# Performance work log

Measured on AMD Instinct MI355X. Metric: run time of the kernel, lower is better.

The kernel has to match this reference:

```python
import jax, jax.numpy as jnp
import numpy as np

N = 100000
E = 1600000
D_IN = 128
HEADS = 8
HEAD_DIM = 16  # hidden_channels // heads = 128 // 8
D_HID = HEADS * HEAD_DIM  # 128
D_OUT = 128
NEG_SLOPE = 0.2


def setup_inputs() -> dict:
    key = jax.random.key(0)
    ks = jax.random.split(key, 10)
    x = jax.random.normal(ks[0], (N, D_IN), dtype=jnp.float32)
    edge_index = jax.random.randint(ks[1], (2, E), 0, N, dtype=jnp.int64)
    s = 1.0 / np.sqrt(D_IN)
    W_gat = jax.random.uniform(ks[2], (D_IN, D_HID), minval=-s, maxval=s, dtype=jnp.float32)
    att_src = jax.random.uniform(ks[3], (HEADS, HEAD_DIM), minval=-s, maxval=s, dtype=jnp.float32)
    att_dst = jax.random.uniform(ks[4], (HEADS, HEAD_DIM), minval=-s, maxval=s, dtype=jnp.float32)
    b_gat = jnp.zeros((D_HID,), dtype=jnp.float32)
    so = 1.0 / np.sqrt(D_OUT)
    W_fc1 = jax.random.uniform(ks[5], (D_OUT, D_OUT), minval=-so, maxval=so, dtype=jnp.float32)
    b_fc1 = jax.random.uniform(ks[6], (D_OUT,), minval=-so, maxval=so, dtype=jnp.float32)
    W_fc2 = jax.random.uniform(ks[7], (D_OUT, D_OUT), minval=-so, maxval=so, dtype=jnp.float32)
    b_fc2 = jax.random.uniform(ks[8], (D_OUT,), minval=-so, maxval=so, dtype=jnp.float32)
    return {"x": x, "edge_index": edge_index, "W_gat": W_gat, "att_src": att_src,
            "att_dst": att_dst, "b_gat": b_gat, "W_fc1": W_fc1, "b_fc1": b_fc1,
            "W_fc2": W_fc2, "b_fc2": b_fc2}


def _gat_conv(x, src, dst, W_gat, att_src, att_dst, b_gat):
    n = x.shape[0]
    xp = (x @ W_gat).reshape(n, HEADS, HEAD_DIM)        # [N,H,C]
    a_src = jnp.einsum('nhc,hc->nh', xp, att_src)       # [N,H]
    a_dst = jnp.einsum('nhc,hc->nh', xp, att_dst)       # [N,H]
    e = jax.nn.leaky_relu(a_src[src] + a_dst[dst], NEG_SLOPE)  # [E,H]
    # segment softmax over edges grouped by destination node
    e_max = jax.ops.segment_max(e, dst, num_segments=n)
    e = jnp.exp(e - e_max[dst])
    e_sum = jax.ops.segment_sum(e, dst, num_segments=n)
    alpha = e / (e_sum[dst] + 1e-16)                    # [E,H]
    msg = xp[src] * alpha[:, :, None]                   # [E,H,C]
    out = jax.ops.segment_sum(msg, dst, num_segments=n) # [N,H,C]
    return out.reshape(n, D_HID) + b_gat


def reference(x, edge_index, W_gat, att_src, att_dst, b_gat, W_fc1, b_fc1, W_fc2, b_fc2):
    n = x.shape[0]
    # PyG GATConv default add_self_loops=True
    loops = jnp.arange(n, dtype=edge_index.dtype)
    src = jnp.concatenate([edge_index[0], loops])
    dst = jnp.concatenate([edge_index[1], loops])
    z = _gat_conv(x, src, dst, W_gat, att_src, att_dst, b_gat)
    z1 = z @ W_fc1 + b_fc1
    z2 = z @ W_fc2 + b_fc2
    return (z, z1, z2)
```

## Files before the change

kernel.cpp:

```cpp
#include <hip/hip_runtime.h>
#include <hip/hip_bf16.h>


#define NBUCK  256
#define BSHIFT 9
#define BNODES 512
#define IPB    8192

typedef __attribute__((ext_vector_type(8))) short bf16x8;
typedef __attribute__((ext_vector_type(4))) float f32x4;

static __device__ __forceinline__ short f2bf(float f) {
    __hip_bfloat16 h = __float2bfloat16(f);
    return *reinterpret_cast<short*>(&h);
}

__global__ __launch_bounds__(256) void k0_swizzle(
    const float* __restrict__ W0, const float* __restrict__ W1,
    const float* __restrict__ W2, const float* __restrict__ att_s,
    const float* __restrict__ att_d, unsigned short* __restrict__ S0,
    unsigned short* __restrict__ S1, unsigned short* __restrict__ S2,
    unsigned short* __restrict__ Sa)
{
    const int t = blockIdx.x * 256 + threadIdx.x;
    if (t < 3 * 2048) {
        const int m = t >> 11;
        const int r = t & 2047;
        const int tile = r >> 6;
        const int l    = r & 63;
        const int ks   = tile & 3;
        const int cb   = tile >> 2;
        const int c    = cb * 16 + (l & 15);
        const int kb   = ks * 32 + (l >> 4) * 8;
        const float* W = (m == 0) ? W0 : (m == 1) ? W1 : W2;
        unsigned short* S = (m == 0) ? S0 : (m == 1) ? S1 : S2;
        unsigned short* dst = S + ((size_t)tile * 64 + l) * 8;
#pragma unroll
        for (int j = 0; j < 8; ++j)
            dst[j] = (unsigned short)f2bf(W[(kb + j) * 128 + c]);
    } else if (t < 3 * 2048 + 256) {
        const int r  = t - 3 * 2048;
        const int ks = r >> 6;
        const int l  = r & 63;
        const int hp = l & 15;
        const int h  = hp & 7;
        const float* av = (hp < 8) ? (att_s + h * 16) : (att_d + h * 16);
        unsigned short* dst = Sa + ((size_t)ks * 64 + l) * 8;
#pragma unroll
        for (int j = 0; j < 8; ++j) {
            const int k = ks * 32 + (l >> 4) * 8 + j;
            float acc = 0.f;
#pragma unroll
            for (int u = 0; u < 16; ++u)
                acc += W0[k * 128 + h * 16 + u] * av[u];
            dst[j] = (unsigned short)f2bf(acc);
        }
    }
}

__global__ __launch_bounds__(256) void g1_mfma(
    const float* __restrict__ x, const unsigned short* __restrict__ Wswz,
    const unsigned short* __restrict__ Sa, unsigned short* __restrict__ xpb,
    float* __restrict__ a_src, float* __restrict__ a_dst, int n)
{
    const int wid  = __builtin_amdgcn_readfirstlane(threadIdx.x >> 6);
    const int lane = threadIdx.x & 63;
    const int lr   = lane & 15;
    const int kg   = lane >> 4;
    const int rowbase = blockIdx.x * 128 + wid * 32;

    bf16x8 afr[2][4];
#pragma unroll
    for (int rt = 0; rt < 2; ++rt) {
        int row = rowbase + rt * 16 + lr;
        row = (row < n) ? row : (n - 1);
        const float* rp = x + (size_t)row * 128 + kg * 8;
#pragma unroll
        for (int ks = 0; ks < 4; ++ks) {
            const float4 v0 = *reinterpret_cast<const float4*>(rp + ks * 32);
            const float4 v1 = *reinterpret_cast<const float4*>(rp + ks * 32 + 4);
            bf16x8 a;
            a[0] = f2bf(v0.x); a[1] = f2bf(v0.y); a[2] = f2bf(v0.z); a[3] = f2bf(v0.w);
            a[4] = f2bf(v1.x); a[5] = f2bf(v1.y); a[6] = f2bf(v1.z); a[7] = f2bf(v1.w);
            afr[rt][ks] = a;
        }
    }

    f32x4 acc[2][8] = {};
#pragma unroll
    for (int cb = 0; cb < 8; ++cb) {
        const unsigned short* bp = Wswz + ((size_t)(cb * 4) * 64 + lane) * 8;
        bf16x8 bfr[4];
#pragma unroll
        for (int ks = 0; ks < 4; ++ks)
            bfr[ks] = *reinterpret_cast<const bf16x8*>(bp + (size_t)ks * 512);
#pragma unroll
        for (int ks = 0; ks < 4; ++ks) {
            acc[0][cb] = __builtin_amdgcn_mfma_f32_16x16x32_bf16(afr[0][ks], bfr[ks], acc[0][cb], 0, 0, 0);
            acc[1][cb] = __builtin_amdgcn_mfma_f32_16x16x32_bf16(afr[1][ks], bfr[ks], acc[1][cb], 0, 0, 0);
        }
    }

    f32x4 accs[2] = {};
#pragma unroll
    for (int ks = 0; ks < 4; ++ks) {
        const bf16x8 bs = *reinterpret_cast<const bf16x8*>(Sa + ((size_t)ks * 64 + lane) * 8);
        accs[0] = __builtin_amdgcn_mfma_f32_16x16x32_bf16(afr[0][ks], bs, accs[0], 0, 0, 0);
        accs[1] = __builtin_amdgcn_mfma_f32_16x16x32_bf16(afr[1][ks], bs, accs[1], 0, 0, 0);
    }

#pragma unroll
    for (int rt = 0; rt < 2; ++rt) {
#pragma unroll
        for (int reg = 0; reg < 4; ++reg) {
            const int row = rowbase + rt * 16 + kg * 4 + reg;
            if (row < n) {
                unsigned short* op = xpb + (size_t)row * 128 + lr;
#pragma unroll
                for (int cb = 0; cb < 8; ++cb)
                    op[cb * 16] = (unsigned short)f2bf(acc[rt][cb][reg]);
                if (lr < 8) a_src[row * 8 + lr] = accs[rt][reg];
                else        a_dst[row * 8 + (lr - 8)] = accs[rt][reg];
            }
        }
    }
}

__global__ __launch_bounds__(256) void p1_hist(
    const int* __restrict__ ei, int* __restrict__ M, int E, int N, int nblk)
{
    __shared__ int h[NBUCK];
    const int tid = threadIdx.x;
    for (int k = tid; k < NBUCK; k += 256) h[k] = 0;
    __syncthreads();

    const int tot = E + N;
    const int base = blockIdx.x * IPB;
    const int lim = (base + IPB < tot) ? base + IPB : tot;
    for (int j = base + tid; j < lim; j += 256) {
        const int d = (j < E) ? ei[E + j] : (j - E);
        atomicAdd(&h[d >> BSHIFT], 1);
    }
    __syncthreads();
    for (int k = tid; k < NBUCK; k += 256)
        M[(size_t)k * nblk + blockIdx.x] = h[k];
}

__global__ __launch_bounds__(256) void p2a_colscan(
    int* __restrict__ M, int* __restrict__ col_total, int nblk)
{
    const int b    = blockIdx.x;
    const int tid  = threadIdx.x;
    const int lane = tid & 63;
    const int wid  = tid >> 6;
    __shared__ int wsum[4];

    int carry = 0;
    for (int base = 0; base < nblk; base += 256) {
        const int idx = base + tid;
        const int v = (idx < nblk) ? M[(size_t)b * nblk + idx] : 0;
        int ws = v;
#pragma unroll
        for (int off = 1; off < 64; off <<= 1) {
            const int t = __shfl_up(ws, off);
            if (lane >= off) ws += t;
        }
        if (lane == 63) wsum[wid] = ws;
        __syncthreads();
        int woff = 0;
        for (int w2 = 0; w2 < wid; ++w2) woff += wsum[w2];
        const int alltot = wsum[0] + wsum[1] + wsum[2] + wsum[3];
        if (idx < nblk) M[(size_t)b * nblk + idx] = carry + woff + ws - v;
        carry += alltot;
        __syncthreads();
    }
    if (tid == 0) col_total[b] = carry;
}

__global__ __launch_bounds__(NBUCK) void p2b_bucketptr(
    const int* __restrict__ col_total, int* __restrict__ bucket_ptr,
    int* __restrict__ row_ptr, int N)
{
    const int tid  = threadIdx.x;
    const int lane = tid & 63;
    const int wid  = tid >> 6;
    __shared__ int wsum[4];

    const int v = col_total[tid];
    int ws = v;
#pragma unroll
    for (int off = 1; off < 64; off <<= 1) {
        const int t = __shfl_up(ws, off);
        if (lane >= off) ws += t;
    }
    if (lane == 63) wsum[wid] = ws;
    __syncthreads();
    int woff = 0;
    for (int w2 = 0; w2 < wid; ++w2) woff += wsum[w2];
    const int excl = woff + ws - v;
    bucket_ptr[tid] = excl;
    if (tid == NBUCK - 1) {
        bucket_ptr[NBUCK] = excl + v;
        row_ptr[N] = excl + v;
    }
}

__global__ __launch_bounds__(256) void p3_scatter(
    const int* __restrict__ ei, const int* __restrict__ M,
    const int* __restrict__ bucket_ptr, int* __restrict__ pairs,
    int E, int N, int nblk)
{
    __shared__ int lcnt[NBUCK];
    const int tid = threadIdx.x;
    for (int k = tid; k < NBUCK; k += 256) lcnt[k] = 0;
    __syncthreads();

    const int tot = E + N;
    const int base = blockIdx.x * IPB;
    const int lim = (base + IPB < tot) ? base + IPB : tot;
    for (int j = base + tid; j < lim; j += 256) {
        int s, d;
        if (j < E) { s = ei[j]; d = ei[E + j]; }
        else       { s = j - E; d = s; }
        const int b = d >> BSHIFT;
        const int r = atomicAdd(&lcnt[b], 1);
        const int pos = bucket_ptr[b] + M[(size_t)b * nblk + blockIdx.x] + r;
        pairs[pos] = s | ((d & (BNODES - 1)) << 17);
    }
}

__global__ __launch_bounds__(256) void p4_finalize(
    const int* __restrict__ pairs, const int* __restrict__ bucket_ptr,
    int* __restrict__ row_ptr, int* __restrict__ csr_src, int N)
{
    const int b     = blockIdx.x;
    const int node0 = b << BSHIFT;
    const int beg   = bucket_ptr[b];
    const int end   = bucket_ptr[b + 1];
    const int tid   = threadIdx.x;
    const int lane  = tid & 63;
    const int wid   = tid >> 6;

    __shared__ int hist[BNODES];
    __shared__ int exc[BNODES];
    __shared__ int cnt2[BNODES];
    __shared__ int wsum[4];

    for (int k = tid; k < BNODES; k += 256) { hist[k] = 0; cnt2[k] = 0; }
    __syncthreads();

    for (int i = beg + tid; i < end; i += 256)
        atomicAdd(&hist[pairs[i] >> 17], 1);
    __syncthreads();

    const int a0 = hist[2 * tid];
    const int a1 = hist[2 * tid + 1];
    const int s  = a0 + a1;
    int ws = s;
#pragma unroll
    for (int off = 1; off < 64; off <<= 1) {
        const int t = __shfl_up(ws, off);
        if (lane >= off) ws += t;
    }
    if (lane == 63) wsum[wid] = ws;
    __syncthreads();
    int woff = 0;
    for (int w2 = 0; w2 < wid; ++w2) woff += wsum[w2];
    const int e0 = woff + ws - s;
    exc[2 * tid]     = e0;
    exc[2 * tid + 1] = e0 + a0;
    __syncthreads();

    for (int k = tid; k < BNODES; k += 256) {
        const int node = node0 + k;
        if (node < N) row_ptr[node] = beg + exc[k];
    }
    for (int i = beg + tid; i < end; i += 256) {
        const int v  = pairs[i];
        const int dl = v >> 17;
        const int r  = atomicAdd(&cnt2[dl], 1);
        csr_src[beg + exc[dl] + r] = v & 0x1FFFF;
    }
}

__global__ __launch_bounds__(256) void k5_aggregate(
    const unsigned short* __restrict__ xpb, const float* __restrict__ a_src,
    const float* __restrict__ a_dst, const int* __restrict__ row_ptr,
    const int* __restrict__ csr_src, const float* __restrict__ b_gat,
    float* __restrict__ z, unsigned int* __restrict__ zb, int n)
{
    const int wave = blockIdx.x * 4 + __builtin_amdgcn_readfirstlane(threadIdx.x >> 6);
    if (wave >= n) return;
    const int lane = threadIdx.x & 63;
    const int d = wave;
    const int beg = row_ptr[d];
    const int end = row_ptr[d + 1];
    const int h = lane >> 3;
    const float adst = a_dst[d * 8 + h];
    const int co = 2 * lane;

    float l0 = 0.f, l1 = 0.f;
    float ax0 = 0.f, ay0 = 0.f, ax1 = 0.f, ay1 = 0.f;

    int i = beg;
    for (; i + 4 <= end; i += 4) {
        const int s0 = csr_src[i + 0];
        const int s1 = csr_src[i + 1];
        const int s2 = csr_src[i + 2];
        const int s3 = csr_src[i + 3];
        const unsigned int xv0 = *reinterpret_cast<const unsigned int*>(xpb + (size_t)s0 * 128 + co);
        const unsigned int xv1 = *reinterpret_cast<const unsigned int*>(xpb + (size_t)s1 * 128 + co);
        const unsigned int xv2 = *reinterpret_cast<const unsigned int*>(xpb + (size_t)s2 * 128 + co);
        const unsigned int xv3 = *reinterpret_cast<const unsigned int*>(xpb + (size_t)s3 * 128 + co);
        float v0 = a_src[s0 * 8 + h] + adst;
        float v1 = a_src[s1 * 8 + h] + adst;
        float v2 = a_src[s2 * 8 + h] + adst;
        float v3 = a_src[s3 * 8 + h] + adst;
        v0 = (v0 > 0.f) ? v0 : 0.2f * v0;
        v1 = (v1 > 0.f) ? v1 : 0.2f * v1;
        v2 = (v2 > 0.f) ? v2 : 0.2f * v2;
        v3 = (v3 > 0.f) ? v3 : 0.2f * v3;
        const float p0 = __expf(v0);
        const float p1 = __expf(v1);
        const float p2 = __expf(v2);
        const float p3 = __expf(v3);
        l0 += p0 + p1;
        l1 += p2 + p3;
        ax0 = fmaf(p0, __uint_as_float(xv0 << 16), ax0);
        ay0 = fmaf(p0, __uint_as_float(xv0 & 0xffff0000u), ay0);
        ax1 = fmaf(p1, __uint_as_float(xv1 << 16), ax1);
        ay1 = fmaf(p1, __uint_as_float(xv1 & 0xffff0000u), ay1);
        ax0 = fmaf(p2, __uint_as_float(xv2 << 16), ax0);
        ay0 = fmaf(p2, __uint_as_float(xv2 & 0xffff0000u), ay0);
        ax1 = fmaf(p3, __uint_as_float(xv3 << 16), ax1);
        ay1 = fmaf(p3, __uint_as_float(xv3 & 0xffff0000u), ay1);
    }
    for (; i < end; ++i) {
        const int s = csr_src[i];
        const unsigned int xv = *reinterpret_cast<const unsigned int*>(xpb + (size_t)s * 128 + co);
        float v = a_src[s * 8 + h] + adst;
        v = (v > 0.f) ? v : 0.2f * v;
        const float p = __expf(v);
        l0 += p;
        ax0 = fmaf(p, __uint_as_float(xv << 16), ax0);
        ay0 = fmaf(p, __uint_as_float(xv & 0xffff0000u), ay0);
    }

    const float inv = 1.0f / (l0 + l1 + 1e-16f);
    const float2 bg = *reinterpret_cast<const float2*>(&b_gat[co]);
    float2 o;
    o.x = (ax0 + ax1) * inv + bg.x;
    o.y = (ay0 + ay1) * inv + bg.y;
    *reinterpret_cast<float2*>(&z[(size_t)d * 128 + co]) = o;
    const unsigned int pk = ((unsigned int)(unsigned short)f2bf(o.y) << 16) |
                            (unsigned int)(unsigned short)f2bf(o.x);
    zb[(size_t)d * 64 + lane] = pk;
}

__global__ __launch_bounds__(256) void g2_mfma_fc(
    const unsigned int* __restrict__ zb,
    const unsigned short* __restrict__ S1, const unsigned short* __restrict__ S2,
    const float* __restrict__ b1, const float* __restrict__ b2,
    float* __restrict__ z1, float* __restrict__ z2, int n)
{
    const int wid  = __builtin_amdgcn_readfirstlane(threadIdx.x >> 6);
    const int lane = threadIdx.x & 63;
    const int lr   = lane & 15;
    const int kg   = lane >> 4;
    const int rowbase = blockIdx.x * 128 + wid * 32;

    bf16x8 afr[2][4];
#pragma unroll
    for (int rt = 0; rt < 2; ++rt) {
        int row = rowbase + rt * 16 + lr;
        row = (row < n) ? row : (n - 1);
        const unsigned short* rp = (const unsigned short*)(zb + (size_t)row * 64) + kg * 8;
#pragma unroll
        for (int ks = 0; ks < 4; ++ks)
            afr[rt][ks] = *reinterpret_cast<const bf16x8*>(rp + ks * 32);
    }

    f32x4 acc1[2][8] = {};
    f32x4 acc2[2][8] = {};
#pragma unroll
    for (int cb = 0; cb < 8; ++cb) {
        const unsigned short* bp1 = S1 + ((size_t)(cb * 4) * 64 + lane) * 8;
        const unsigned short* bp2 = S2 + ((size_t)(cb * 4) * 64 + lane) * 8;
        bf16x8 f1[4], f2v[4];
#pragma unroll
        for (int ks = 0; ks < 4; ++ks) {
            f1[ks]  = *reinterpret_cast<const bf16x8*>(bp1 + (size_t)ks * 512);
            f2v[ks] = *reinterpret_cast<const bf16x8*>(bp2 + (size_t)ks * 512);
        }
#pragma unroll
        for (int ks = 0; ks < 4; ++ks) {
            acc1[0][cb] = __builtin_amdgcn_mfma_f32_16x16x32_bf16(afr[0][ks], f1[ks],  acc1[0][cb], 0, 0, 0);
            acc1[1][cb] = __builtin_amdgcn_mfma_f32_16x16x32_bf16(afr[1][ks], f1[ks],  acc1[1][cb], 0, 0, 0);
            acc2[0][cb] = __builtin_amdgcn_mfma_f32_16x16x32_bf16(afr[0][ks], f2v[ks], acc2[0][cb], 0, 0, 0);
            acc2[1][cb] = __builtin_amdgcn_mfma_f32_16x16x32_bf16(afr[1][ks], f2v[ks], acc2[1][cb], 0, 0, 0);
        }
    }

    float bb1[8], bb2[8];
#pragma unroll
    for (int cb = 0; cb < 8; ++cb) { bb1[cb] = b1[cb * 16 + lr]; bb2[cb] = b2[cb * 16 + lr]; }

#pragma unroll
    for (int rt = 0; rt < 2; ++rt) {
#pragma unroll
        for (int reg = 0; reg < 4; ++reg) {
            const int row = rowbase + rt * 16 + kg * 4 + reg;
            if (row < n) {
                float* o1 = z1 + (size_t)row * 128 + lr;
                float* o2 = z2 + (size_t)row * 128 + lr;
#pragma unroll
                for (int cb = 0; cb < 8; ++cb) {
                    o1[cb * 16] = acc1[rt][cb][reg] + bb1[cb];
                    o2[cb * 16] = acc2[rt][cb][reg] + bb2[cb];
                }
            }
        }
    }
}

extern "C" void kernel_launch(void* const* d_in, const int* in_sizes, int n_in,
                              void* d_out, int out_size, void* d_ws, size_t ws_size,
                              hipStream_t stream)
{
    const float* x       = (const float*)d_in[0];
    const int*   ei      = (const int*)  d_in[1];
    const float* W_gat   = (const float*)d_in[2];
    const float* att_src = (const float*)d_in[3];
    const float* att_dst = (const float*)d_in[4];
    const float* b_gat   = (const float*)d_in[5];
    const float* W_fc1   = (const float*)d_in[6];
    const float* b_fc1   = (const float*)d_in[7];
    const float* W_fc2   = (const float*)d_in[8];
    const float* b_fc2   = (const float*)d_in[9];

    const int N = in_sizes[0] / 128;
    const int E = in_sizes[1] / 2;
    const int tot = E + N;
    const int nblk = (tot + IPB - 1) / IPB;
    const int nbuck_used = (N + BNODES - 1) >> BSHIFT;

    char* w = (char*)d_ws;
    unsigned short* xpb = (unsigned short*)w;  w += (size_t)N * 128 * 2;
    unsigned int* zb = (unsigned int*)w;       w += (size_t)N * 64 * 4;
    float* a_src  = (float*)w;  w += (size_t)N * 8 * 4;
    float* a_dst  = (float*)w;  w += (size_t)N * 8 * 4;
    int* row_ptr  = (int*)w;    w += (size_t)(N + 1) * 4;
    w = (char*)(((size_t)w + 15) & ~(size_t)15);
    unsigned short* S0 = (unsigned short*)w; w += 16384 * 2;
    unsigned short* S1 = (unsigned short*)w; w += 16384 * 2;
    unsigned short* S2 = (unsigned short*)w; w += 16384 * 2;
    unsigned short* Sa = (unsigned short*)w; w += 2048 * 2;
    int* M          = (int*)w;  w += (size_t)nblk * NBUCK * 4;
    int* col_total  = (int*)w;  w += NBUCK * 4;
    int* bucket_ptr = (int*)w;  w += (NBUCK + 1) * 4;
    w = (char*)(((size_t)w + 15) & ~(size_t)15);
    int* pairs    = (int*)w;    w += (size_t)tot * 4;
    int* csr_src  = (int*)w;    w += (size_t)tot * 4;

    float* z  = (float*)d_out;
    float* z1 = z  + (size_t)N * 128;
    float* z2 = z1 + (size_t)N * 128;

    k0_swizzle<<<(3 * 2048 + 256 + 255) / 256, 256, 0, stream>>>(
        W_gat, W_fc1, W_fc2, att_src, att_dst, S0, S1, S2, Sa);

    g1_mfma<<<(N + 127) / 128, 256, 0, stream>>>(x, S0, Sa, xpb, a_src, a_dst, N);

    p1_hist<<<nblk, 256, 0, stream>>>(ei, M, E, N, nblk);
    p2a_colscan<<<NBUCK, 256, 0, stream>>>(M, col_total, nblk);
    p2b_bucketptr<<<1, NBUCK, 0, stream>>>(col_total, bucket_ptr, row_ptr, N);
    p3_scatter<<<nblk, 256, 0, stream>>>(ei, M, bucket_ptr, pairs, E, N, nblk);
    p4_finalize<<<nbuck_used, 256, 0, stream>>>(pairs, bucket_ptr, row_ptr, csr_src, N);

    k5_aggregate<<<(N + 3) / 4, 256, 0, stream>>>(xpb, a_src, a_dst, row_ptr, csr_src,
                                                  b_gat, z, zb, N);

    g2_mfma_fc<<<(N + 127) / 128, 256, 0, stream>>>(zb, S1, S2, b_fc1, b_fc2, z1, z2, N);
}
```

Measured before the change: 218.7 us.

## Merge projection GEMM with edge histogram and fold bucket-pointer scan into column scan

The projection GEMM and the destination-bucket histogram now run in a single launch, with blocks split by index. The histogram accumulates per-bucket totals atomically into col_total, which k0 zeroes, so the column scan can compute bucket offsets itself. That lets it write absolute positions, and the separate bucket-pointer kernel is removed. The aggregation loop is also rewritten to batch 8 neighbor loads with clamped indices, exposing more memory-level parallelism. The cost is some redundant work: every scan block recomputes the 256-entry prefix, and tail iterations do masked loads.

```diff
diff --git a/kernel.cpp b/kernel.cpp
--- a/kernel.cpp
+++ b/kernel.cpp
@@ -20,9 +20,10 @@
     const float* __restrict__ W2, const float* __restrict__ att_s,
     const float* __restrict__ att_d, unsigned short* __restrict__ S0,
     unsigned short* __restrict__ S1, unsigned short* __restrict__ S2,
-    unsigned short* __restrict__ Sa)
+    unsigned short* __restrict__ Sa, int* __restrict__ col_total)
 {
     const int t = blockIdx.x * 256 + threadIdx.x;
+    if (t < NBUCK) col_total[t] = 0;
     if (t < 3 * 2048) {
         const int m = t >> 11;
         const int r = t & 2047;
@@ -58,106 +59,133 @@
     }
 }
 
-__global__ __launch_bounds__(256) void g1_mfma(
+__global__ __launch_bounds__(256) void g1p1(
     const float* __restrict__ x, const unsigned short* __restrict__ Wswz,
     const unsigned short* __restrict__ Sa, unsigned short* __restrict__ xpb,
-    float* __restrict__ a_src, float* __restrict__ a_dst, int n)
-{
-    const int wid  = __builtin_amdgcn_readfirstlane(threadIdx.x >> 6);
-    const int lane = threadIdx.x & 63;
-    const int lr   = lane & 15;
-    const int kg   = lane >> 4;
-    const int rowbase = blockIdx.x * 128 + wid * 32;
-
-    bf16x8 afr[2][4];
-#pragma unroll
-    for (int rt = 0; rt < 2; ++rt) {
-        int row = rowbase + rt * 16 + lr;
-        row = (row < n) ? row : (n - 1);
-        const float* rp = x + (size_t)row * 128 + kg * 8;
+    float* __restrict__ a_src, float* __restrict__ a_dst,
+    const int* __restrict__ ei, int* __restrict__ M, int* __restrict__ col_total,
+    int n, int E, int g1b, int nblk)
+{
+    if ((int)blockIdx.x < g1b) {
+        const int wid  = __builtin_amdgcn_readfirstlane(threadIdx.x >> 6);
+        const int lane = threadIdx.x & 63;
+        const int lr   = lane & 15;
+        const int kg   = lane >> 4;
+        const int rowbase = blockIdx.x * 128 + wid * 32;
+
+        bf16x8 afr[2][4];
+#pragma unroll
+        for (int rt = 0; rt < 2; ++rt) {
+            int row = rowbase + rt * 16 + lr;
+            row = (row < n) ? row : (n - 1);
+            const float* rp = x + (size_t)row * 128 + kg * 8;
+#pragma unroll
+            for (int ks = 0; ks < 4; ++ks) {
+                const float4 v0 = *reinterpret_cast<const float4*>(rp + ks * 32);
+                const float4 v1 = *reinterpret_cast<const float4*>(rp + ks * 32 + 4);
+                bf16x8 a;
+                a[0] = f2bf(v0.x); a[1] = f2bf(v0.y); a[2] = f2bf(v0.z); a[3] = f2bf(v0.w);
+                a[4] = f2bf(v1.x); a[5] = f2bf(v1.y); a[6] = f2bf(v1.z); a[7] = f2bf(v1.w);
+                afr[rt][ks] = a;
+            }
+        }
+
+        f32x4 acc[2][8] = {};
+#pragma unroll
+        for (int cb = 0; cb < 8; ++cb) {
+            const unsigned short* bp = Wswz + ((size_t)(cb * 4) * 64 + lane) * 8;
+            bf16x8 bfr[4];
+#pragma unroll
+            for (int ks = 0; ks < 4; ++ks)
+                bfr[ks] = *reinterpret_cast<const bf16x8*>(bp + (size_t)ks * 512);
+#pragma unroll
+            for (int ks = 0; ks < 4; ++ks) {
+                acc[0][cb] = __builtin_amdgcn_mfma_f32_16x16x32_bf16(afr[0][ks], bfr[ks], acc[0][cb], 0, 0, 0);
+                acc[1][cb] = __builtin_amdgcn_mfma_f32_16x16x32_bf16(afr[1][ks], bfr[ks], acc[1][cb], 0, 0, 0);
+            }
+        }
+
+        f32x4 accs[2] = {};
 #pragma unroll
         for (int ks = 0; ks < 4; ++ks) {
-            const float4 v0 = *reinterpret_cast<const float4*>(rp + ks * 32);
-            const float4 v1 = *reinterpret_cast<const float4*>(rp + ks * 32 + 4);
-            bf16x8 a;
-            a[0] = f2bf(v0.x); a[1] = f2bf(v0.y); a[2] = f2bf(v0.z); a[3] = f2bf(v0.w);
-            a[4] = f2bf(v1.x); a[5] = f2bf(v1.y); a[6] = f2bf(v1.z); a[7] = f2bf(v1.w);
-            afr[rt][ks] = a;
-        }
-    }
-
-    f32x4 acc[2][8] = {};
-#pragma unroll
-    for (int cb = 0; cb < 8; ++cb) {
-        const unsigned short* bp = Wswz + ((size_t)(cb * 4) * 64 + lane) * 8;
-        bf16x8 bfr[4];
-#pragma unroll
-        for (int ks = 0; ks < 4; ++ks)
-            bfr[ks] = *reinterpret_cast<const bf16x8*>(bp + (size_t)ks * 512);
-#pragma unroll
-        for (int ks = 0; ks < 4; ++ks) {
-            acc[0][cb] = __builtin_amdgcn_mfma_f32_16x16x32_bf16(afr[0][ks], bfr[ks], acc[0][cb], 0, 0, 0);
-            acc[1][cb] = __builtin_amdgcn_mfma_f32_16x16x32_bf16(afr[1][ks], bfr[ks], acc[1][cb], 0, 0, 0);
-        }
-    }
-
-    f32x4 accs[2] = {};
-#pragma unroll
-    for (int ks = 0; ks < 4; ++ks) {
-        const bf16x8 bs = *reinterpret_cast<const bf16x8*>(Sa + ((size_t)ks * 64 + lane) * 8);
-        accs[0] = __builtin_amdgcn_mfma_f32_16x16x32_bf16(afr[0][ks], bs, accs[0], 0, 0, 0);
-        accs[1] = __builtin_amdgcn_mfma_f32_16x16x32_bf16(afr[1][ks], bs, accs[1], 0, 0, 0);
-    }
-
-#pragma unroll
-    for (int rt = 0; rt < 2; ++rt) {
-#pragma unroll
-        for (int reg = 0; reg < 4; ++reg) {
-            const int row = rowbase + rt * 16 + kg * 4 + reg;
-            if (row < n) {
-                unsigned short* op = xpb + (size_t)row * 128 + lr;
-#pragma unroll
-                for (int cb = 0; cb < 8; ++cb)
-                    op[cb * 16] = (unsigned short)f2bf(acc[rt][cb][reg]);
-                if (lr < 8) a_src[row * 8 + lr] = accs[rt][reg];
-                else        a_dst[row * 8 + (lr - 8)] = accs[rt][reg];
+            const bf16x8 bs = *reinterpret_cast<const bf16x8*>(Sa + ((size_t)ks * 64 + lane) * 8);
+            accs[0] = __builtin_amdgcn_mfma_f32_16x16x32_bf16(afr[0][ks], bs, accs[0], 0, 0, 0);
+            accs[1] = __builtin_amdgcn_mfma_f32_16x16x32_bf16(afr[1][ks], bs, accs[1], 0, 0, 0);
+        }
+
+#pragma unroll
+        for (int rt = 0; rt < 2; ++rt) {
+#pragma unroll
+            for (int reg = 0; reg < 4; ++reg) {
+                const int row = rowbase + rt * 16 + kg * 4 + reg;
+                if (row < n) {
+                    unsigned short* op = xpb + (size_t)row * 128 + lr;
+#pragma unroll
+                    for (int cb = 0; cb < 8; ++cb)
+                        op[cb * 16] = (unsigned short)f2bf(acc[rt][cb][reg]);
+                    if (lr < 8) a_src[row * 8 + lr] = accs[rt][reg];
+                    else        a_dst[row * 8 + (lr - 8)] = accs[rt][reg];
+                }
             }
         }
-    }
-}
-
-__global__ __launch_bounds__(256) void p1_hist(
-    const int* __restrict__ ei, int* __restrict__ M, int E, int N, int nblk)
-{
-    __shared__ int h[NBUCK];
-    const int tid = threadIdx.x;
-    for (int k = tid; k < NBUCK; k += 256) h[k] = 0;
-    __syncthreads();
-
-    const int tot = E + N;
-    const int base = blockIdx.x * IPB;
-    const int lim = (base + IPB < tot) ? base + IPB : tot;
-    for (int j = base + tid; j < lim; j += 256) {
-        const int d = (j < E) ? ei[E + j] : (j - E);
-        atomicAdd(&h[d >> BSHIFT], 1);
-    }
-    __syncthreads();
-    for (int k = tid; k < NBUCK; k += 256)
-        M[(size_t)k * nblk + blockIdx.x] = h[k];
+    } else {
+        __shared__ int h[NBUCK];
+        const int pb  = blockIdx.x - g1b;
+        const int tid = threadIdx.x;
+        for (int k = tid; k < NBUCK; k += 256) h[k] = 0;
+        __syncthreads();
+
+        const int tot = E + n;
+        const int base = pb * IPB;
+        const int lim = (base + IPB < tot) ? base + IPB : tot;
+        for (int j = base + tid; j < lim; j += 256) {
+            const int d = (j < E) ? ei[E + j] : (j - E);
+            atomicAdd(&h[d >> BSHIFT], 1);
+        }
+        __syncthreads();
+        for (int k = tid; k < NBUCK; k += 256) {
+            M[(size_t)k * nblk + pb] = h[k];
+            if (h[k]) atomicAdd(&col_total[k], h[k]);
+        }
+    }
 }
 
 __global__ __launch_bounds__(256) void p2a_colscan(
-    int* __restrict__ M, int* __restrict__ col_total, int nblk)
+    int* __restrict__ M, const int* __restrict__ col_total,
+    int* __restrict__ bucket_ptr, int* __restrict__ row_ptr, int nblk, int N)
 {
     const int b    = blockIdx.x;
     const int tid  = threadIdx.x;
     const int lane = tid & 63;
     const int wid  = tid >> 6;
     __shared__ int wsum[4];
-
-    int carry = 0;
-    for (int base = 0; base < nblk; base += 256) {
-        const int idx = base + tid;
+    __shared__ int sbase;
+
+    const int v0 = col_total[tid];
+    int ws0 = v0;
+#pragma unroll
+    for (int off = 1; off < 64; off <<= 1) {
+        const int t = __shfl_up(ws0, off);
+        if (lane >= off) ws0 += t;
+    }
+    if (lane == 63) wsum[wid] = ws0;
+    __syncthreads();
+    int woff0 = 0;
+    for (int w2 = 0; w2 < wid; ++w2) woff0 += wsum[w2];
+    const int excl0 = woff0 + ws0 - v0;
+    if (tid == b) sbase = excl0;
+    if (b == NBUCK - 1 && tid == NBUCK - 1) {
+        bucket_ptr[NBUCK] = excl0 + v0;
+        row_ptr[N] = excl0 + v0;
+    }
+    __syncthreads();
+    const int base = sbase;
+    if (tid == 0) bucket_ptr[b] = base;
+    __syncthreads();
+
+    int carry = base;
+    for (int bb = 0; bb < nblk; bb += 256) {
+        const int idx = bb + tid;
         const int v = (idx < nblk) ? M[(size_t)b * nblk + idx] : 0;
         int ws = v;
 #pragma unroll
@@ -174,41 +202,11 @@
         carry += alltot;
         __syncthreads();
     }
-    if (tid == 0) col_total[b] = carry;
-}
-
-__global__ __launch_bounds__(NBUCK) void p2b_bucketptr(
-    const int* __restrict__ col_total, int* __restrict__ bucket_ptr,
-    int* __restrict__ row_ptr, int N)
-{
-    const int tid  = threadIdx.x;
-    const int lane = tid & 63;
-    const int wid  = tid >> 6;
-    __shared__ int wsum[4];
-
-    const int v = col_total[tid];
-    int ws = v;
-#pragma unroll
-    for (int off = 1; off < 64; off <<= 1) {
-        const int t = __shfl_up(ws, off);
-        if (lane >= off) ws += t;
-    }
-    if (lane == 63) wsum[wid] = ws;
-    __syncthreads();
-    int woff = 0;
-    for (int w2 = 0; w2 < wid; ++w2) woff += wsum[w2];
-    const int excl = woff + ws - v;
-    bucket_ptr[tid] = excl;
-    if (tid == NBUCK - 1) {
-        bucket_ptr[NBUCK] = excl + v;
-        row_ptr[N] = excl + v;
-    }
 }
 
 __global__ __launch_bounds__(256) void p3_scatter(
     const int* __restrict__ ei, const int* __restrict__ M,
-    const int* __restrict__ bucket_ptr, int* __restrict__ pairs,
-    int E, int N, int nblk)
+    int* __restrict__ pairs, int E, int N, int nblk)
 {
     __shared__ int lcnt[NBUCK];
     const int tid = threadIdx.x;
@@ -224,7 +222,7 @@
         else       { s = j - E; d = s; }
         const int b = d >> BSHIFT;
         const int r = atomicAdd(&lcnt[b], 1);
-        const int pos = bucket_ptr[b] + M[(size_t)b * nblk + blockIdx.x] + r;
+        const int pos = M[(size_t)b * nblk + blockIdx.x] + r;
         pairs[pos] = s | ((d & (BNODES - 1)) << 17);
     }
 }
@@ -302,48 +300,39 @@
     float l0 = 0.f, l1 = 0.f;
     float ax0 = 0.f, ay0 = 0.f, ax1 = 0.f, ay1 = 0.f;
 
-    int i = beg;
-    for (; i + 4 <= end; i += 4) {
-        const int s0 = csr_src[i + 0];
-        const int s1 = csr_src[i + 1];
-        const int s2 = csr_src[i + 2];
-        const int s3 = csr_src[i + 3];
-        const unsigned int xv0 = *reinterpret_cast<const unsigned int*>(xpb + (size_t)s0 * 128 + co);
-        const unsigned int xv1 = *reinterpret_cast<const unsigned int*>(xpb + (size_t)s1 * 128 + co);
-        const unsigned int xv2 = *reinterpret_cast<const unsigned int*>(xpb + (size_t)s2 * 128 + co);
-        const unsigned int xv3 = *reinterpret_cast<const unsigned int*>(xpb + (size_t)s3 * 128 + co);
-        float v0 = a_src[s0 * 8 + h] + adst;
-        float v1 = a_src[s1 * 8 + h] + adst;
-        float v2 = a_src[s2 * 8 + h] + adst;
-        float v3 = a_src[s3 * 8 + h] + adst;
-        v0 = (v0 > 0.f) ? v0 : 0.2f * v0;
-        v1 = (v1 > 0.f) ? v1 : 0.2f * v1;
-        v2 = (v2 > 0.f) ? v2 : 0.2f * v2;
-        v3 = (v3 > 0.f) ? v3 : 0.2f * v3;
-        const float p0 = __expf(v0);
-        const float p1 = __expf(v1);
-        const float p2 = __expf(v2);
-        const float p3 = __expf(v3);
-        l0 += p0 + p1;
-        l1 += p2 + p3;
-        ax0 = fmaf(p0, __uint_as_float(xv0 << 16), ax0);
-        ay0 = fmaf(p0, __uint_as_float(xv0 & 0xffff0000u), ay0);
-        ax1 = fmaf(p1, __uint_as_float(xv1 << 16), ax1);
-        ay1 = fmaf(p1, __uint_as_float(xv1 & 0xffff0000u), ay1);
-        ax0 = fmaf(p2, __uint_as_float(xv2 << 16), ax0);
-        ay0 = fmaf(p2, __uint_as_float(xv2 & 0xffff0000u), ay0);
-        ax1 = fmaf(p3, __uint_as_float(xv3 << 16), ax1);
-        ay1 = fmaf(p3, __uint_as_float(xv3 & 0xffff0000u), ay1);
-    }
-    for (; i < end; ++i) {
-        const int s = csr_src[i];
-        const unsigned int xv = *reinterpret_cast<const unsigned int*>(xpb + (size_t)s * 128 + co);
-        float v = a_src[s * 8 + h] + adst;
-        v = (v > 0.f) ? v : 0.2f * v;
-        const float p = __expf(v);
-        l0 += p;
-        ax0 = fmaf(p, __uint_as_float(xv << 16), ax0);
-        ay0 = fmaf(p, __uint_as_float(xv & 0xffff0000u), ay0);
+    for (int i = beg; i < end; i += 8) {
+        int ss[8];
+        unsigned int xv[8];
+        float pv[8];
+#pragma unroll
+        for (int j = 0; j < 8; ++j) {
+            const int idx = i + j;
+            ss[j] = csr_src[(idx < end) ? idx : (end - 1)];
+        }
+#pragma unroll
+        for (int j = 0; j < 8; ++j)
+            xv[j] = *reinterpret_cast<const unsigned int*>(xpb + (size_t)ss[j] * 128 + co);
+#pragma unroll
+        for (int j = 0; j < 8; ++j) {
+            float v = a_src[ss[j] * 8 + h] + adst;
+            v = (v > 0.f) ? v : 0.2f * v;
+            const float e = __expf(v);
+            pv[j] = (i + j < end) ? e : 0.f;
+        }
+#pragma unroll
+        for (int j = 0; j < 8; ++j) {
+            const float cx = __uint_as_float(xv[j] << 16);
+            const float cy = __uint_as_float(xv[j] & 0xffff0000u);
+            if (j & 1) {
+                l1 += pv[j];
+                ax1 = fmaf(pv[j], cx, ax1);
+                ay1 = fmaf(pv[j], cy, ay1);
+            } else {
+                l0 += pv[j];
+                ax0 = fmaf(pv[j], cx, ax0);
+                ay0 = fmaf(pv[j], cy, ay0);
+            }
+        }
     }
 
     const float inv = 1.0f / (l0 + l1 + 1e-16f);
@@ -443,6 +432,7 @@
     const int tot = E + N;
     const int nblk = (tot + IPB - 1) / IPB;
     const int nbuck_used = (N + BNODES - 1) >> BSHIFT;
+    const int g1b = (N + 127) / 128;
 
     char* w = (char*)d_ws;
     unsigned short* xpb = (unsigned short*)w;  w += (size_t)N * 128 * 2;
@@ -467,14 +457,13 @@
     float* z2 = z1 + (size_t)N * 128;
 
     k0_swizzle<<<(3 * 2048 + 256 + 255) / 256, 256, 0, stream>>>(
-        W_gat, W_fc1, W_fc2, att_src, att_dst, S0, S1, S2, Sa);
-
-    g1_mfma<<<(N + 127) / 128, 256, 0, stream>>>(x, S0, Sa, xpb, a_src, a_dst, N);
-
-    p1_hist<<<nblk, 256, 0, stream>>>(ei, M, E, N, nblk);
-    p2a_colscan<<<NBUCK, 256, 0, stream>>>(M, col_total, nblk);
-    p2b_bucketptr<<<1, NBUCK, 0, stream>>>(col_total, bucket_ptr, row_ptr, N);
-    p3_scatter<<<nblk, 256, 0, stream>>>(ei, M, bucket_ptr, pairs, E, N, nblk);
+        W_gat, W_fc1, W_fc2, att_src, att_dst, S0, S1, S2, Sa, col_total);
+
+    g1p1<<<g1b + nblk, 256, 0, stream>>>(x, S0, Sa, xpb, a_src, a_dst,
+                                         ei, M, col_total, N, E, g1b, nblk);
+
+    p2a_colscan<<<NBUCK, 256, 0, stream>>>(M, col_total, bucket_ptr, row_ptr, nblk, N);
+    p3_scatter<<<nblk, 256, 0, stream>>>(ei, M, pairs, E, N, nblk);
     p4_finalize<<<nbuck_used, 256, 0, stream>>>(pairs, bucket_ptr, row_ptr, csr_src, N);
 
     k5_aggregate<<<(N + 3) / 4, 256, 0, stream>>>(xpb, a_src, a_dst, row_ptr, csr_src,
```

Result: faster. 204.8 us (-6.4%).
